# Performance work log

Hardware: AMD Instinct MI355X
Metric: run time of the kernel (lower is better)

## Reference

```python
import jax, jax.numpy as jnp
import numpy as np

B, S, HID = 1, 2048, 2048
H, KV, D = 16, 4, 128
N_REP = H // KV
WINDOW = 1024
THETA = 10000.0
EPS = 1e-6
SCALE = D ** -0.5


def setup_inputs() -> dict:
    key = jax.random.key(0)
    ks = jax.random.split(key, 10)
    s = 0.02
    return {
        "hidden_states": jax.random.normal(ks[0], (B, S, HID), jnp.float32),
        "Wq": jax.random.normal(ks[1], (HID, H * D), jnp.float32) * s,
        "bq": jnp.zeros((H * D,), jnp.float32),
        "Wk": jax.random.normal(ks[2], (HID, KV * D), jnp.float32) * s,
        "bk": jnp.zeros((KV * D,), jnp.float32),
        "Wv": jax.random.normal(ks[3], (HID, KV * D), jnp.float32) * s,
        "bv": jnp.zeros((KV * D,), jnp.float32),
        "Wo": jax.random.normal(ks[4], (H * D, HID), jnp.float32) * s,
        "memory_gate": jnp.zeros((1, H, 1, 1), jnp.float32),
    }


def _rope_tables(seq_len, dim, dtype):
    inv_freq = 1.0 / (THETA ** (jnp.arange(0, dim, 2, dtype=jnp.float32) / dim))
    t = jnp.arange(seq_len, dtype=jnp.float32)
    freqs = t[:, None] * inv_freq[None, :]          # [S, D/2]
    emb = jnp.concatenate([freqs, freqs], axis=-1)  # [S, D]
    return jnp.cos(emb).astype(dtype), jnp.sin(emb).astype(dtype)


def _rotate_half(x):
    x1, x2 = x[..., : x.shape[-1] // 2], x[..., x.shape[-1] // 2 :]
    return jnp.concatenate([-x2, x1], axis=-1)


def reference(hidden_states, Wq, bq, Wk, bk, Wv, bv, Wo, memory_gate):
    b, s, _ = hidden_states.shape
    q = (hidden_states @ Wq + bq).reshape(b, s, H, D).transpose(0, 2, 1, 3)   # [B,H,S,D]
    k = (hidden_states @ Wk + bk).reshape(b, s, KV, D).transpose(0, 2, 1, 3)  # [B,KV,S,D]
    v = (hidden_states @ Wv + bv).reshape(b, s, KV, D).transpose(0, 2, 1, 3)

    cos, sin = _rope_tables(s, D, q.dtype)  # [S,D]
    cos = cos[None, None]                   # [1,1,S,D]
    sin = sin[None, None]
    q_rot = q * cos + _rotate_half(q) * sin
    k_rot = k * cos + _rotate_half(k) * sin

    # GQA repeat of rotated K and raw V to H heads
    k_rep = jnp.repeat(k_rot, N_REP, axis=1)  # [B,H,S,D]
    v_rep = jnp.repeat(v, N_REP, axis=1)

    # sliding-window causal attention (seq_len > window path)
    scores = jnp.einsum("bhsd,bhtd->bhst", q_rot, k_rep) * SCALE
    row = jnp.arange(s)[:, None]
    col = jnp.arange(s)[None, :]
    mask = (col <= row) & (row - col < WINDOW)  # [S,S]
    scores = jnp.where(mask[None, None], scores, -jnp.inf)
    probs = jax.nn.softmax(scores.astype(jnp.float32), axis=-1).astype(q.dtype)
    local = jnp.einsum("bhst,bhtd->bhsd", probs, v_rep)

    # infini-memory retrieval: memory is reset before retrieve, so M=0, z=0
    sigma_q = jax.nn.elu(q) + 1.0                        # unrotated (NoPE) query
    M = jnp.zeros((b, H, D, D), q.dtype)
    z = jnp.zeros((b, H, D), q.dtype)
    num = jnp.einsum("bhsd,bhde->bhse", sigma_q, M)
    den = jnp.einsum("bhsd,bhd->bhs", sigma_q, z) + EPS
    global_out = num / den[..., None]                    # zeros, but faithful math

    gate = jax.nn.sigmoid(memory_gate)                   # [1,H,1,1]
    out = gate * global_out + (1.0 - gate) * local       # [B,H,S,D]
    out = out.transpose(0, 2, 1, 3).reshape(b, s, H * D)
    return out @ Wo
```

## Files before the change

### kernel.cpp

```cpp
#include <hip/hip_runtime.h>
#include <stdint.h>

typedef __attribute__((ext_vector_type(8))) short short8;
typedef __attribute__((ext_vector_type(4))) float f32x4;

#define S_LEN 2048
#define HID 2048
#define NH 16
#define NKV 4
#define DH 128
#define WINDOW 1024
#define SCALE 0.08838834764831845f

__device__ __forceinline__ unsigned short f2bf(float f) {
    unsigned int u = __float_as_uint(f);
    unsigned int r = (u + 0x7fffu + ((u >> 16) & 1u)) >> 16;
    return (unsigned short)r;
}

__device__ __forceinline__ float bf2f(unsigned short u) {
    return __uint_as_float((unsigned int)u << 16);
}

__device__ __forceinline__ void gload16(const void* g, void* l) {
    __builtin_amdgcn_global_load_lds((__attribute__((address_space(1))) void*)g,
                                     (__attribute__((address_space(3))) void*)l, 16, 0, 0);
}


__global__ __launch_bounds__(256) void cast4_kernel(const float* __restrict__ src,
                                                    unsigned short* __restrict__ dst, int n4) {
    int i = blockIdx.x * 256 + threadIdx.x;
    if (i < n4) {
        float4 v = ((const float4*)src)[i];
        ushort4 o;
        o.x = f2bf(v.x); o.y = f2bf(v.y); o.z = f2bf(v.z); o.w = f2bf(v.w);
        ((ushort4*)dst)[i] = o;
    }
}

__global__ __launch_bounds__(256) void build_bias_kernel(const float* __restrict__ bq,
                                                         const float* __restrict__ bk,
                                                         const float* __restrict__ bv,
                                                         float* __restrict__ cbias) {
    int i = blockIdx.x * 256 + threadIdx.x;
    if (i < 3072) {
        float v;
        if (i < 2048) v = bq[i];
        else if (i < 2560) v = bk[i - 2048];
        else v = bv[i - 2560];
        cbias[i] = v;
    }
}

__global__ __launch_bounds__(256) void transpose_cast_kernel(const float* __restrict__ src,
                                                             unsigned short* __restrict__ dst,
                                                             int N, int K, int rowoff) {
    __shared__ unsigned short t[32][33];
    int n0 = blockIdx.x * 32, k0 = blockIdx.y * 32;
    int c = threadIdx.x & 31, r8 = threadIdx.x >> 5;
#pragma unroll
    for (int i = 0; i < 4; i++) {
        int r = r8 + i * 8;
        t[r][c] = f2bf(src[(size_t)(k0 + r) * N + n0 + c]);
    }
    __syncthreads();
#pragma unroll
    for (int i = 0; i < 4; i++) {
        int r = r8 + i * 8;
        dst[(size_t)(rowoff + n0 + r) * K + k0 + c] = t[c][r];
    }
}


template <bool BF16OUT>
__global__ __launch_bounds__(256) void gemm_pipe(const unsigned short* __restrict__ A,
                                                 const unsigned short* __restrict__ Bt,
                                                 void* __restrict__ Cv,
                                                 const float* __restrict__ bias,
                                                 int M, int N, int K) {
    __shared__ unsigned short Al[3][128 * 32];
    __shared__ unsigned short Bl[3][128 * 32];
    const int tid = threadIdx.x, lane = tid & 63, w = tid >> 6;
    const int lo = lane & 15, hi = lane >> 4;
    const int nbn = N >> 7;
    const int nwg8 = gridDim.x >> 3;
    const int wg = (blockIdx.x & 7) * nwg8 + (blockIdx.x >> 3);
    const int bm = wg / nbn, bn = wg % nbn;
    const int m0 = bm << 7, n0 = bn << 7;
    const int wr = w >> 1, wc = w & 1;
    const size_t Kb = (size_t)K * 2;

    const char* Ab = (const char*)A + (size_t)m0 * Kb;
    const char* Bb = (const char*)Bt + (size_t)n0 * Kb;
    char* Alb = (char*)&Al[0][0];
    char* Blb = (char*)&Bl[0][0];

    const int L0 = tid * 16;
    const int L1 = 4096 + tid * 16;
    const int r0 = L0 >> 6, r1 = L1 >> 6;
    const size_t go0 = (size_t)r0 * Kb + ((((L0 >> 4) & 3) ^ (r0 & 3)) << 4);
    const size_t go1 = (size_t)r1 * Kb + ((((L1 >> 4) & 3) ^ (r1 & 3)) << 4);

    auto stage = [&](int buf, int kt) {
        const char* Ak = Ab + (size_t)kt * 64;
        const char* Bk = Bb + (size_t)kt * 64;
        char* Ad = Alb + buf * 8192;
        char* Bd = Blb + buf * 8192;
        gload16(Ak + go0, Ad + L0);
        gload16(Ak + go1, Ad + L1);
        gload16(Bk + go0, Bd + L0);
        gload16(Bk + go1, Bd + L1);
    };

    f32x4 acc[4][4] = {};
    const int NT = K >> 5;
    const int swz = (hi ^ (lo & 3)) << 4;

    stage(0, 0);
    stage(1, 1);
    int buf = 0, nstage = 2;
    for (int kt = 0; kt < NT; ++kt) {
        if (kt < NT - 1)
            asm volatile("s_waitcnt vmcnt(4)" ::: "memory");
        else
            asm volatile("s_waitcnt vmcnt(0)" ::: "memory");
        __builtin_amdgcn_s_barrier();

        const char* Ar = Alb + buf * 8192;
        const char* Br = Blb + buf * 8192;
        short8 af[4], bfr[4];
#pragma unroll
        for (int m = 0; m < 4; m++)
            af[m] = *(const short8*)(Ar + (wr * 64 + m * 16 + lo) * 64 + swz);
#pragma unroll
        for (int n = 0; n < 4; n++)
            bfr[n] = *(const short8*)(Br + (wc * 64 + n * 16 + lo) * 64 + swz);
        asm volatile("s_waitcnt lgkmcnt(0)" ::: "memory");
        __builtin_amdgcn_s_barrier();

        if (kt + 2 < NT) {
            int bst = nstage;
            bst = (bst >= 3) ? bst - 3 : bst;
            stage(bst, kt + 2);
            nstage = bst + 1;
        }
        __builtin_amdgcn_sched_barrier(0);

        __builtin_amdgcn_s_setprio(1);
#pragma unroll
        for (int m = 0; m < 4; m++)
#pragma unroll
            for (int n = 0; n < 4; n++)
                acc[m][n] = __builtin_amdgcn_mfma_f32_16x16x32_bf16(af[m], bfr[n], acc[m][n], 0, 0, 0);
        __builtin_amdgcn_s_setprio(0);

        buf = (buf == 2) ? 0 : buf + 1;
    }

#pragma unroll
    for (int m = 0; m < 4; m++) {
        const int row = m0 + wr * 64 + m * 16 + hi * 4;
#pragma unroll
        for (int n = 0; n < 4; n++) {
            const int col = n0 + wc * 64 + n * 16 + lo;
            const float badd = bias ? bias[col] : 0.f;
#pragma unroll
            for (int r = 0; r < 4; r++) {
                const float v = acc[m][n][r] + badd;
                if constexpr (BF16OUT)
                    ((unsigned short*)Cv)[(size_t)(row + r) * N + col] = f2bf(v);
                else
                    ((float*)Cv)[(size_t)(row + r) * N + col] = v;
            }
        }
    }
}

__global__ __launch_bounds__(256) void rope_qk_kernel(const unsigned short* __restrict__ qkv,
                                                      unsigned short* __restrict__ Qr,
                                                      unsigned short* __restrict__ Kr) {
    int s = blockIdx.x, tid = threadIdx.x;
    __shared__ float cs[64], sn[64];
    if (tid < 64) {
        float inv = __expf(-(float)tid * (logf(10000.f) / 64.f));
        float ang = (float)s * inv;
        float si, co;
        sincosf(ang, &si, &co);
        cs[tid] = co;
        sn[tid] = si;
    }
    __syncthreads();
    const unsigned short* row = qkv + (size_t)s * 3072;
#pragma unroll
    for (int it = 0; it < 8; ++it) {
        int j = tid + it * 256;
        int h = j >> 7, d = j & 127, f = d & 63;
        float x = bf2f(row[j]);
        float other = bf2f(row[(j & ~127) + (d ^ 64)]);
        float v = (d < 64) ? x * cs[f] - other * sn[f] : x * cs[f] + other * sn[f];
        Qr[((size_t)h * S_LEN + s) * 128 + d] = f2bf(v);
    }
#pragma unroll
    for (int it = 0; it < 2; ++it) {
        int j = tid + it * 256;
        int kvh = j >> 7, d = j & 127, f = d & 63;
        float x = bf2f(row[2048 + j]);
        float other = bf2f(row[2048 + (j & ~127) + (d ^ 64)]);
        float v = (d < 64) ? x * cs[f] - other * sn[f] : x * cs[f] + other * sn[f];
        Kr[((size_t)kvh * S_LEN + s) * 128 + d] = f2bf(v);
    }
}

__global__ __launch_bounds__(256) void transpose_v_kernel(const unsigned short* __restrict__ qkv,
                                                          unsigned short* __restrict__ Vt) {
    __shared__ unsigned short t[128][132];
    const int s0 = blockIdx.x * 128;
    const int kvh = blockIdx.y;
    const int tx = threadIdx.x & 15, ty = threadIdx.x >> 4;
    const unsigned short* src = qkv + 2560 + kvh * 128;
#pragma unroll
    for (int i = 0; i < 8; i++) {
        const int sl = ty + i * 16;
        short8 v = *(const short8*)(src + (size_t)(s0 + sl) * 3072 + tx * 8);
#pragma unroll
        for (int j = 0; j < 8; j++) t[sl][tx * 8 + j] = v[j];
    }
    __syncthreads();
    unsigned short* dst = Vt + (size_t)kvh * 128 * S_LEN + s0;
#pragma unroll
    for (int i = 0; i < 8; i++) {
        const int d = ty + i * 16;
        short8 v;
#pragma unroll
        for (int j = 0; j < 8; j++) v[j] = t[tx * 8 + j][d];
        *(short8*)(dst + (size_t)d * S_LEN + tx * 8) = v;
    }
}


__global__ __launch_bounds__(256) void attn_kernel(const unsigned short* __restrict__ Qr,
                                                   const unsigned short* __restrict__ Kr,
                                                   const unsigned short* __restrict__ Vt,
                                                   const float* __restrict__ mg,
                                                   unsigned short* __restrict__ Ao) {
    __shared__ unsigned short Kl[2][64 * 128];
    __shared__ unsigned short Vl[2][128 * 64];
    __shared__ unsigned short Pl[4][16 * 64];
    const int tid = threadIdx.x, lane = tid & 63, w = tid >> 6;
    const int h = blockIdx.y, qt = blockIdx.x;
    const int kvh = h >> 2;
    const int q0 = qt * 64;
    const int lo = lane & 15, hi = lane >> 4;

    const unsigned short* Qb =
        Qr + ((size_t)h * S_LEN + q0 + w * 16 + lo) * 128 + hi * 8;
    short8 qf[4];
#pragma unroll
    for (int ks = 0; ks < 4; ++ks) qf[ks] = *(const short8*)(Qb + ks * 32);

    const float gate = 1.f / (1.f + __expf(-mg[h]));
    const float fac = 1.f - gate;

    float mrow[4] = {-INFINITY, -INFINITY, -INFINITY, -INFINITY};
    float lrow[4] = {0.f, 0.f, 0.f, 0.f};
    f32x4 o[8] = {};

    const char* Kg = (const char*)(Kr + (size_t)kvh * S_LEN * 128);
    const char* Vg = (const char*)(Vt + (size_t)kvh * 128 * S_LEN);
    char* Klb = (char*)&Kl[0][0];
    char* Vlb = (char*)&Vl[0][0];
    const int wb = w * 1024;

    auto stage = [&](int buf, int kt) {
        const int k0 = kt * 64;
#pragma unroll
        for (int iss = 0; iss < 4; ++iss) {
            int lin = iss * 4096 + tid * 16;
            int row = lin >> 8;
            int chunk = (lin >> 4) & 15;
            gload16(Kg + (size_t)(k0 + row) * 256 + ((chunk ^ (row & 7)) << 4),
                    Klb + buf * 16384 + iss * 4096 + wb);
            int d = lin >> 7;
            int vchunk = (lin >> 4) & 7;
            gload16(Vg + (size_t)d * (S_LEN * 2) + (size_t)k0 * 2 + ((vchunk ^ (d & 7)) << 4),
                    Vlb + buf * 16384 + iss * 4096 + wb);
        }
    };

    const int qmin = q0 + w * 16;
    const int t0 = (q0 >= 1023) ? (q0 - 1023) >> 6 : 0;
    stage(0, t0);
    for (int kt = t0; kt <= qt; ++kt) {
        __syncthreads();
        if (kt < qt) stage((kt - t0 + 1) & 1, kt + 1);
        const int buf = (kt - t0) & 1;
        const int k0 = kt * 64;
        const char* Kb = Klb + buf * 16384;
        const char* Vb = Vlb + buf * 16384;

        f32x4 sc[4];
        __builtin_amdgcn_s_setprio(1);
#pragma unroll
        for (int t = 0; t < 4; t++) {
            sc[t] = (f32x4){0.f, 0.f, 0.f, 0.f};
            const int krow = t * 16 + lo;
#pragma unroll
            for (int ks = 0; ks < 4; ks++) {
                const int chunk = ks * 4 + hi;
                short8 kf = *(const short8*)(Kb + krow * 256 + ((chunk ^ (krow & 7)) << 4));
                sc[t] = __builtin_amdgcn_mfma_f32_16x16x32_bf16(qf[ks], kf, sc[t], 0, 0, 0);
            }
        }
        __builtin_amdgcn_s_setprio(0);

        const bool full = (k0 + 63 <= qmin) && (k0 >= qmin + 15 - (WINDOW - 1));
        float ps[4][4];
        float mt[4];
        if (full) {
#pragma unroll
            for (int r = 0; r < 4; r++) {
                float m0v = -INFINITY;
#pragma unroll
                for (int t = 0; t < 4; t++) {
                    float sv = sc[t][r] * SCALE;
                    ps[t][r] = sv;
                    m0v = fmaxf(m0v, sv);
                }
                mt[r] = m0v;
            }
        } else {
#pragma unroll
            for (int r = 0; r < 4; r++) {
                const int q = qmin + hi * 4 + r;
                float m0v = -INFINITY;
#pragma unroll
                for (int t = 0; t < 4; t++) {
                    const int k = k0 + t * 16 + lo;
                    const bool valid = (k <= q) && (q - k < WINDOW);
                    float sv = valid ? sc[t][r] * SCALE : -INFINITY;
                    ps[t][r] = sv;
                    m0v = fmaxf(m0v, sv);
                }
                mt[r] = m0v;
            }
        }

        float alpha[4];
        bool need = false;
#pragma unroll
        for (int r = 0; r < 4; r++) {
#pragma unroll
            for (int off = 1; off < 16; off <<= 1) mt[r] = fmaxf(mt[r], __shfl_xor(mt[r], off, 64));
            const float mo = mrow[r];
            const float mn = (mt[r] > mo + 8.f) ? mt[r] : mo;
            const bool resc = (mn != mo);
            alpha[r] = resc ? __expf(mo - mn) : 1.f;
            need = need || resc;
            mrow[r] = mn;
            const float mn_e = (mn == -INFINITY) ? 0.f : mn;
            float ls = 0.f;
#pragma unroll
            for (int t = 0; t < 4; t++) {
                float p = __expf(ps[t][r] - mn_e);
                ps[t][r] = p;
                ls += p;
            }
#pragma unroll
            for (int off = 1; off < 16; off <<= 1) ls += __shfl_xor(ls, off, 64);
            lrow[r] = lrow[r] * alpha[r] + ls;
        }

        char* Pw = (char*)&Pl[w][0];
#pragma unroll
        for (int r = 0; r < 4; r++) {
            const int prow = hi * 4 + r;
#pragma unroll
            for (int t = 0; t < 4; t++) {
                const int col = t * 16 + lo;
                const int chunk = col >> 3;
                *(unsigned short*)(Pw + prow * 128 + ((chunk ^ (prow & 7)) << 4) + (col & 7) * 2) =
                    f2bf(ps[t][r]);
            }
        }
        asm volatile("s_waitcnt lgkmcnt(0)" ::: "memory");
        __builtin_amdgcn_sched_barrier(0);

        if (__any(need)) {
#pragma unroll
            for (int n = 0; n < 8; n++)
#pragma unroll
                for (int r = 0; r < 4; r++) o[n][r] *= alpha[r];
        }

        short8 pa[2];
#pragma unroll
        for (int ks = 0; ks < 2; ++ks) {
            const int chunk = ks * 4 + hi;
            pa[ks] = *(const short8*)(Pw + lo * 128 + ((chunk ^ (lo & 7)) << 4));
        }

        __builtin_amdgcn_s_setprio(1);
#pragma unroll
        for (int n = 0; n < 8; n++) {
            const int d = n * 16 + lo;
#pragma unroll
            for (int ks = 0; ks < 2; ++ks) {
                const int chunk = ks * 4 + hi;
                short8 vbf = *(const short8*)(Vb + d * 128 + ((chunk ^ (d & 7)) << 4));
                o[n] = __builtin_amdgcn_mfma_f32_16x16x32_bf16(pa[ks], vbf, o[n], 0, 0, 0);
            }
        }
        __builtin_amdgcn_s_setprio(0);
        __syncthreads();
    }

#pragma unroll
    for (int r = 0; r < 4; r++) {
        const int s = q0 + w * 16 + hi * 4 + r;
        const float inv = fac / lrow[r];
#pragma unroll
        for (int n = 0; n < 8; n++) {
            const int d = n * 16 + lo;
            Ao[(size_t)s * 2048 + h * 128 + d] = f2bf(o[n][r] * inv);
        }
    }
}


extern "C" void kernel_launch(void* const* d_in, const int* in_sizes, int n_in,
                              void* d_out, int out_size, void* d_ws, size_t ws_size,
                              hipStream_t stream) {
    const float* hs = (const float*)d_in[0];
    const float* Wq = (const float*)d_in[1];
    const float* bq = (const float*)d_in[2];
    const float* Wk = (const float*)d_in[3];
    const float* bk = (const float*)d_in[4];
    const float* Wv = (const float*)d_in[5];
    const float* bv = (const float*)d_in[6];
    const float* Wo = (const float*)d_in[7];
    const float* mg = (const float*)d_in[8];

    char* ws = (char*)d_ws;
    unsigned short* hsb   = (unsigned short*)(ws + 0);
    unsigned short* woT   = (unsigned short*)(ws + 0);
    unsigned short* wqkvT = (unsigned short*)(ws + 8388608);
    unsigned short* attnb = (unsigned short*)(ws + 8388608);
    unsigned short* qkvb  = (unsigned short*)(ws + 20971520);
    unsigned short* Qrb   = (unsigned short*)(ws + 33554432);
    unsigned short* Krb   = (unsigned short*)(ws + 41943040);
    unsigned short* Vtb   = (unsigned short*)(ws + 44040192);
    float*          cbias = (float*)(ws + 46137344);

    cast4_kernel<<<4096, 256, 0, stream>>>(hs, hsb, 1048576);
    build_bias_kernel<<<12, 256, 0, stream>>>(bq, bk, bv, cbias);
    transpose_cast_kernel<<<dim3(64, 64), 256, 0, stream>>>(Wq, wqkvT, 2048, 2048, 0);
    transpose_cast_kernel<<<dim3(16, 64), 256, 0, stream>>>(Wk, wqkvT, 512, 2048, 2048);
    transpose_cast_kernel<<<dim3(16, 64), 256, 0, stream>>>(Wv, wqkvT, 512, 2048, 2560);

    gemm_pipe<true><<<16 * 24, 256, 0, stream>>>(hsb, wqkvT, qkvb, cbias, 2048, 3072, 2048);

    transpose_cast_kernel<<<dim3(64, 64), 256, 0, stream>>>(Wo, woT, 2048, 2048, 0);

    rope_qk_kernel<<<2048, 256, 0, stream>>>(qkvb, Qrb, Krb);
    transpose_v_kernel<<<dim3(16, 4), 256, 0, stream>>>(qkvb, Vtb);

    attn_kernel<<<dim3(32, 16), 256, 0, stream>>>(Qrb, Krb, Vtb, mg, attnb);

    gemm_pipe<false><<<16 * 16, 256, 0, stream>>>(attnb, woT, (float*)d_out, nullptr, 2048, 2048, 2048);
}
```

Baseline: 254.5 us.

## Merge prep kernels and fuse RoPE and V transpose into QKV GEMM epilogue

All the casting, bias-gathering and weight-transposing kernels are merged into one prep kernel, which also precomputes RoPE cos/sin tables. The QKV GEMM warp layout changes so each warp owns full 128-wide head columns. This lets its epilogue apply bias and RoPE directly, writing rotated Q/K and transposed V, and removes the intermediate qkv buffer plus two kernels. In attention, the softmax row sum is now computed by an MFMA against a ones vector instead of shuffle reductions. The trade-offs are more register pressure in the GEMM epilogue, scattered stores, and a changed warp tiling that reloads all B fragments per warp.

```diff
diff --git a/kernel.cpp b/kernel.cpp
--- a/kernel.cpp
+++ b/kernel.cpp
@@ -18,47 +18,19 @@
     return (unsigned short)r;
 }
 
-__device__ __forceinline__ float bf2f(unsigned short u) {
-    return __uint_as_float((unsigned int)u << 16);
-}
-
 __device__ __forceinline__ void gload16(const void* g, void* l) {
     __builtin_amdgcn_global_load_lds((__attribute__((address_space(1))) void*)g,
                                      (__attribute__((address_space(3))) void*)l, 16, 0, 0);
 }
 
 
-__global__ __launch_bounds__(256) void cast4_kernel(const float* __restrict__ src,
-                                                    unsigned short* __restrict__ dst, int n4) {
-    int i = blockIdx.x * 256 + threadIdx.x;
-    if (i < n4) {
-        float4 v = ((const float4*)src)[i];
-        ushort4 o;
-        o.x = f2bf(v.x); o.y = f2bf(v.y); o.z = f2bf(v.z); o.w = f2bf(v.w);
-        ((ushort4*)dst)[i] = o;
-    }
-}
-
-__global__ __launch_bounds__(256) void build_bias_kernel(const float* __restrict__ bq,
-                                                         const float* __restrict__ bk,
-                                                         const float* __restrict__ bv,
-                                                         float* __restrict__ cbias) {
-    int i = blockIdx.x * 256 + threadIdx.x;
-    if (i < 3072) {
-        float v;
-        if (i < 2048) v = bq[i];
-        else if (i < 2560) v = bk[i - 2048];
-        else v = bv[i - 2560];
-        cbias[i] = v;
-    }
-}
-
-__global__ __launch_bounds__(256) void transpose_cast_kernel(const float* __restrict__ src,
-                                                             unsigned short* __restrict__ dst,
-                                                             int N, int K, int rowoff) {
-    __shared__ unsigned short t[32][33];
-    int n0 = blockIdx.x * 32, k0 = blockIdx.y * 32;
-    int c = threadIdx.x & 31, r8 = threadIdx.x >> 5;
+__device__ __forceinline__ void tile_transpose(const float* __restrict__ src,
+                                               unsigned short* __restrict__ dst,
+                                               int N, int K, int rowoff, int idx, int nbx,
+                                               unsigned short (*t)[33]) {
+    const int nx = idx & (nbx - 1), ky = idx / nbx;
+    const int n0 = nx * 32, k0 = ky * 32;
+    const int c = threadIdx.x & 31, r8 = threadIdx.x >> 5;
 #pragma unroll
     for (int i = 0; i < 4; i++) {
         int r = r8 + i * 8;
@@ -72,13 +44,58 @@
     }
 }
 
-
-template <bool BF16OUT>
-__global__ __launch_bounds__(256) void gemm_pipe(const unsigned short* __restrict__ A,
-                                                 const unsigned short* __restrict__ Bt,
-                                                 void* __restrict__ Cv,
-                                                 const float* __restrict__ bias,
-                                                 int M, int N, int K) {
+__global__ __launch_bounds__(256) void prep_kernel(
+    const float* __restrict__ hs, unsigned short* __restrict__ hsb,
+    const float* __restrict__ bq, const float* __restrict__ bk, const float* __restrict__ bv,
+    float* __restrict__ cbias, float* __restrict__ cst, float* __restrict__ snt,
+    const float* __restrict__ Wq, const float* __restrict__ Wk,
+    const float* __restrict__ Wv, const float* __restrict__ Wo,
+    unsigned short* __restrict__ wqkvT, unsigned short* __restrict__ woT) {
+    __shared__ unsigned short t[32][33];
+    const int b = blockIdx.x, tid = threadIdx.x;
+    if (b < 4096) {
+        int i = b * 256 + tid;
+        float4 v = ((const float4*)hs)[i];
+        ushort4 o;
+        o.x = f2bf(v.x); o.y = f2bf(v.y); o.z = f2bf(v.z); o.w = f2bf(v.w);
+        ((ushort4*)hsb)[i] = o;
+    } else if (b < 4608) {
+        int idx = (b - 4096) * 256 + tid;
+        int s = idx >> 6, f = idx & 63;
+        float inv = __expf(-(float)f * (logf(10000.f) / 64.f));
+        float ang = (float)s * inv;
+        float si, co;
+        sincosf(ang, &si, &co);
+        cst[idx] = co;
+        snt[idx] = si;
+    } else if (b < 4620) {
+        int i = (b - 4608) * 256 + tid;
+        if (i < 3072) {
+            float v;
+            if (i < 2048) v = bq[i];
+            else if (i < 2560) v = bk[i - 2048];
+            else v = bv[i - 2560];
+            cbias[i] = v;
+        }
+    } else if (b < 8716) {
+        tile_transpose(Wq, wqkvT, 2048, 2048, 0, b - 4620, 64, t);
+    } else if (b < 9740) {
+        tile_transpose(Wk, wqkvT, 512, 2048, 2048, b - 8716, 16, t);
+    } else if (b < 10764) {
+        tile_transpose(Wv, wqkvT, 512, 2048, 2560, b - 9740, 16, t);
+    } else {
+        tile_transpose(Wo, woT, 2048, 2048, 0, b - 10764, 64, t);
+    }
+}
+
+
+template <int EPI>
+__global__ __launch_bounds__(256) void gemm_pipe(
+    const unsigned short* __restrict__ A, const unsigned short* __restrict__ Bt,
+    float* __restrict__ C, const float* __restrict__ bias, int M, int N, int K,
+    unsigned short* __restrict__ Qr, unsigned short* __restrict__ Kr,
+    unsigned short* __restrict__ Vt,
+    const float* __restrict__ cst, const float* __restrict__ snt) {
     __shared__ unsigned short Al[3][128 * 32];
     __shared__ unsigned short Bl[3][128 * 32];
     const int tid = threadIdx.x, lane = tid & 63, w = tid >> 6;
@@ -88,7 +105,6 @@
     const int wg = (blockIdx.x & 7) * nwg8 + (blockIdx.x >> 3);
     const int bm = wg / nbn, bn = wg % nbn;
     const int m0 = bm << 7, n0 = bn << 7;
-    const int wr = w >> 1, wc = w & 1;
     const size_t Kb = (size_t)K * 2;
 
     const char* Ab = (const char*)A + (size_t)m0 * Kb;
@@ -113,7 +129,7 @@
         gload16(Bk + go1, Bd + L1);
     };
 
-    f32x4 acc[4][4] = {};
+    f32x4 acc[2][8] = {};
     const int NT = K >> 5;
     const int swz = (hi ^ (lo & 3)) << 4;
 
@@ -129,13 +145,13 @@
 
         const char* Ar = Alb + buf * 8192;
         const char* Br = Blb + buf * 8192;
-        short8 af[4], bfr[4];
-#pragma unroll
-        for (int m = 0; m < 4; m++)
-            af[m] = *(const short8*)(Ar + (wr * 64 + m * 16 + lo) * 64 + swz);
-#pragma unroll
-        for (int n = 0; n < 4; n++)
-            bfr[n] = *(const short8*)(Br + (wc * 64 + n * 16 + lo) * 64 + swz);
+        short8 af[2], bfr[8];
+#pragma unroll
+        for (int m = 0; m < 2; m++)
+            af[m] = *(const short8*)(Ar + (w * 32 + m * 16 + lo) * 64 + swz);
+#pragma unroll
+        for (int n = 0; n < 8; n++)
+            bfr[n] = *(const short8*)(Br + (n * 16 + lo) * 64 + swz);
         asm volatile("s_waitcnt lgkmcnt(0)" ::: "memory");
         __builtin_amdgcn_s_barrier();
 
@@ -149,92 +165,83 @@
 
         __builtin_amdgcn_s_setprio(1);
 #pragma unroll
-        for (int m = 0; m < 4; m++)
-#pragma unroll
-            for (int n = 0; n < 4; n++)
+        for (int m = 0; m < 2; m++)
+#pragma unroll
+            for (int n = 0; n < 8; n++)
                 acc[m][n] = __builtin_amdgcn_mfma_f32_16x16x32_bf16(af[m], bfr[n], acc[m][n], 0, 0, 0);
         __builtin_amdgcn_s_setprio(0);
 
         buf = (buf == 2) ? 0 : buf + 1;
     }
 
-#pragma unroll
-    for (int m = 0; m < 4; m++) {
-        const int row = m0 + wr * 64 + m * 16 + hi * 4;
-#pragma unroll
-        for (int n = 0; n < 4; n++) {
-            const int col = n0 + wc * 64 + n * 16 + lo;
-            const float badd = bias ? bias[col] : 0.f;
-#pragma unroll
-            for (int r = 0; r < 4; r++) {
-                const float v = acc[m][n][r] + badd;
-                if constexpr (BF16OUT)
-                    ((unsigned short*)Cv)[(size_t)(row + r) * N + col] = f2bf(v);
-                else
-                    ((float*)Cv)[(size_t)(row + r) * N + col] = v;
-            }
-        }
-    }
-}
-
-__global__ __launch_bounds__(256) void rope_qk_kernel(const unsigned short* __restrict__ qkv,
-                                                      unsigned short* __restrict__ Qr,
-                                                      unsigned short* __restrict__ Kr) {
-    int s = blockIdx.x, tid = threadIdx.x;
-    __shared__ float cs[64], sn[64];
-    if (tid < 64) {
-        float inv = __expf(-(float)tid * (logf(10000.f) / 64.f));
-        float ang = (float)s * inv;
-        float si, co;
-        sincosf(ang, &si, &co);
-        cs[tid] = co;
-        sn[tid] = si;
-    }
-    __syncthreads();
-    const unsigned short* row = qkv + (size_t)s * 3072;
-#pragma unroll
-    for (int it = 0; it < 8; ++it) {
-        int j = tid + it * 256;
-        int h = j >> 7, d = j & 127, f = d & 63;
-        float x = bf2f(row[j]);
-        float other = bf2f(row[(j & ~127) + (d ^ 64)]);
-        float v = (d < 64) ? x * cs[f] - other * sn[f] : x * cs[f] + other * sn[f];
-        Qr[((size_t)h * S_LEN + s) * 128 + d] = f2bf(v);
-    }
-#pragma unroll
-    for (int it = 0; it < 2; ++it) {
-        int j = tid + it * 256;
-        int kvh = j >> 7, d = j & 127, f = d & 63;
-        float x = bf2f(row[2048 + j]);
-        float other = bf2f(row[2048 + (j & ~127) + (d ^ 64)]);
-        float v = (d < 64) ? x * cs[f] - other * sn[f] : x * cs[f] + other * sn[f];
-        Kr[((size_t)kvh * S_LEN + s) * 128 + d] = f2bf(v);
-    }
-}
-
-__global__ __launch_bounds__(256) void transpose_v_kernel(const unsigned short* __restrict__ qkv,
-                                                          unsigned short* __restrict__ Vt) {
-    __shared__ unsigned short t[128][132];
-    const int s0 = blockIdx.x * 128;
-    const int kvh = blockIdx.y;
-    const int tx = threadIdx.x & 15, ty = threadIdx.x >> 4;
-    const unsigned short* src = qkv + 2560 + kvh * 128;
-#pragma unroll
-    for (int i = 0; i < 8; i++) {
-        const int sl = ty + i * 16;
-        short8 v = *(const short8*)(src + (size_t)(s0 + sl) * 3072 + tx * 8);
-#pragma unroll
-        for (int j = 0; j < 8; j++) t[sl][tx * 8 + j] = v[j];
-    }
-    __syncthreads();
-    unsigned short* dst = Vt + (size_t)kvh * 128 * S_LEN + s0;
-#pragma unroll
-    for (int i = 0; i < 8; i++) {
-        const int d = ty + i * 16;
-        short8 v;
-#pragma unroll
-        for (int j = 0; j < 8; j++) v[j] = t[tx * 8 + j][d];
-        *(short8*)(dst + (size_t)d * S_LEN + tx * 8) = v;
+    const int sbase = m0 + w * 32 + hi * 4;
+    if constexpr (EPI == 0) {
+#pragma unroll
+        for (int m = 0; m < 2; m++) {
+            const int row = sbase + m * 16;
+#pragma unroll
+            for (int n = 0; n < 8; n++) {
+                const int col = n0 + n * 16 + lo;
+                const float badd = bias ? bias[col] : 0.f;
+#pragma unroll
+                for (int r = 0; r < 4; r++)
+                    C[(size_t)(row + r) * N + col] = acc[m][n][r] + badd;
+            }
+        }
+    } else {
+        if (bn < 20) {
+            float csv[2][4][4], snv[2][4][4];
+#pragma unroll
+            for (int m = 0; m < 2; m++)
+#pragma unroll
+                for (int r = 0; r < 4; r++) {
+                    const int s = sbase + m * 16 + r;
+#pragma unroll
+                    for (int fi = 0; fi < 4; fi++) {
+                        const int f = fi * 16 + lo;
+                        csv[m][r][fi] = cst[s * 64 + f];
+                        snv[m][r][fi] = snt[s * 64 + f];
+                    }
+                }
+            unsigned short* dst = (bn < 16) ? (Qr + (size_t)bn * S_LEN * 128)
+                                            : (Kr + (size_t)(bn - 16) * S_LEN * 128);
+#pragma unroll
+            for (int m = 0; m < 2; m++) {
+#pragma unroll
+                for (int n = 0; n < 8; n++) {
+                    const int d = n * 16 + lo;
+                    const float badd = bias[n0 + d];
+                    const float badd2 = bias[n0 + (d ^ 64)];
+#pragma unroll
+                    for (int r = 0; r < 4; r++) {
+                        const float x = acc[m][n][r] + badd;
+                        const float y = acc[m][n ^ 4][r] + badd2;
+                        const float cs = csv[m][r][n & 3];
+                        const float sn = snv[m][r][n & 3];
+                        const float out = (n < 4) ? x * cs - y * sn : x * cs + y * sn;
+                        const int s = sbase + m * 16 + r;
+                        dst[(size_t)s * 128 + d] = f2bf(out);
+                    }
+                }
+            }
+        } else {
+            const int kvh = bn - 20;
+#pragma unroll
+            for (int m = 0; m < 2; m++) {
+                const int s0r = sbase + m * 16;
+#pragma unroll
+                for (int n = 0; n < 8; n++) {
+                    const int d = n * 16 + lo;
+                    const float badd = bias[n0 + d];
+                    ushort4 pk;
+                    pk.x = f2bf(acc[m][n][0] + badd);
+                    pk.y = f2bf(acc[m][n][1] + badd);
+                    pk.z = f2bf(acc[m][n][2] + badd);
+                    pk.w = f2bf(acc[m][n][3] + badd);
+                    *(ushort4*)(Vt + (size_t)(kvh * 128 + d) * S_LEN + s0r) = pk;
+                }
+            }
+        }
     }
 }
 
@@ -262,9 +269,11 @@
     const float gate = 1.f / (1.f + __expf(-mg[h]));
     const float fac = 1.f - gate;
 
+    const short8 ones = {16256, 16256, 16256, 16256, 16256, 16256, 16256, 16256};
+
     float mrow[4] = {-INFINITY, -INFINITY, -INFINITY, -INFINITY};
-    float lrow[4] = {0.f, 0.f, 0.f, 0.f};
     f32x4 o[8] = {};
+    f32x4 ol = {};
 
     const char* Kg = (const char*)(Kr + (size_t)kvh * S_LEN * 128);
     const char* Vg = (const char*)(Vt + (size_t)kvh * 128 * S_LEN);
@@ -359,16 +368,8 @@
             need = need || resc;
             mrow[r] = mn;
             const float mn_e = (mn == -INFINITY) ? 0.f : mn;
-            float ls = 0.f;
-#pragma unroll
-            for (int t = 0; t < 4; t++) {
-                float p = __expf(ps[t][r] - mn_e);
-                ps[t][r] = p;
-                ls += p;
-            }
-#pragma unroll
-            for (int off = 1; off < 16; off <<= 1) ls += __shfl_xor(ls, off, 64);
-            lrow[r] = lrow[r] * alpha[r] + ls;
+#pragma unroll
+            for (int t = 0; t < 4; t++) ps[t][r] = __expf(ps[t][r] - mn_e);
         }
 
         char* Pw = (char*)&Pl[w][0];
@@ -391,6 +392,8 @@
             for (int n = 0; n < 8; n++)
 #pragma unroll
                 for (int r = 0; r < 4; r++) o[n][r] *= alpha[r];
+#pragma unroll
+            for (int r = 0; r < 4; r++) ol[r] *= alpha[r];
         }
 
         short8 pa[2];
@@ -401,6 +404,8 @@
         }
 
         __builtin_amdgcn_s_setprio(1);
+        ol = __builtin_amdgcn_mfma_f32_16x16x32_bf16(pa[0], ones, ol, 0, 0, 0);
+        ol = __builtin_amdgcn_mfma_f32_16x16x32_bf16(pa[1], ones, ol, 0, 0, 0);
 #pragma unroll
         for (int n = 0; n < 8; n++) {
             const int d = n * 16 + lo;
@@ -418,7 +423,7 @@
 #pragma unroll
     for (int r = 0; r < 4; r++) {
         const int s = q0 + w * 16 + hi * 4 + r;
-        const float inv = fac / lrow[r];
+        const float inv = fac / ol[r];
 #pragma unroll
         for (int n = 0; n < 8; n++) {
             const int d = n * 16 + lo;
@@ -443,29 +448,24 @@
 
     char* ws = (char*)d_ws;
     unsigned short* hsb   = (unsigned short*)(ws + 0);
-    unsigned short* woT   = (unsigned short*)(ws + 0);
+    unsigned short* attnb = (unsigned short*)(ws + 0);
     unsigned short* wqkvT = (unsigned short*)(ws + 8388608);
-    unsigned short* attnb = (unsigned short*)(ws + 8388608);
-    unsigned short* qkvb  = (unsigned short*)(ws + 20971520);
-    unsigned short* Qrb   = (unsigned short*)(ws + 33554432);
-    unsigned short* Krb   = (unsigned short*)(ws + 41943040);
-    unsigned short* Vtb   = (unsigned short*)(ws + 44040192);
-    float*          cbias = (float*)(ws + 46137344);
-
-    cast4_kernel<<<4096, 256, 0, stream>>>(hs, hsb, 1048576);
-    build_bias_kernel<<<12, 256, 0, stream>>>(bq, bk, bv, cbias);
-    transpose_cast_kernel<<<dim3(64, 64), 256, 0, stream>>>(Wq, wqkvT, 2048, 2048, 0);
-    transpose_cast_kernel<<<dim3(16, 64), 256, 0, stream>>>(Wk, wqkvT, 512, 2048, 2048);
-    transpose_cast_kernel<<<dim3(16, 64), 256, 0, stream>>>(Wv, wqkvT, 512, 2048, 2560);
-
-    gemm_pipe<true><<<16 * 24, 256, 0, stream>>>(hsb, wqkvT, qkvb, cbias, 2048, 3072, 2048);
-
-    transpose_cast_kernel<<<dim3(64, 64), 256, 0, stream>>>(Wo, woT, 2048, 2048, 0);
-
-    rope_qk_kernel<<<2048, 256, 0, stream>>>(qkvb, Qrb, Krb);
-    transpose_v_kernel<<<dim3(16, 4), 256, 0, stream>>>(qkvb, Vtb);
+    unsigned short* woT   = (unsigned short*)(ws + 20971520);
+    unsigned short* Qrb   = (unsigned short*)(ws + 29360128);
+    unsigned short* Krb   = (unsigned short*)(ws + 37748736);
+    unsigned short* Vtb   = (unsigned short*)(ws + 39845888);
+    float*          cbias = (float*)(ws + 41943040);
+    float*          cst   = (float*)(ws + 41959424);
+    float*          snt   = (float*)(ws + 42483712);
+
+    prep_kernel<<<14860, 256, 0, stream>>>(hs, hsb, bq, bk, bv, cbias, cst, snt,
+                                           Wq, Wk, Wv, Wo, wqkvT, woT);
+
+    gemm_pipe<1><<<16 * 24, 256, 0, stream>>>(hsb, wqkvT, nullptr, cbias, 2048, 3072, 2048,
+                                              Qrb, Krb, Vtb, cst, snt);
 
     attn_kernel<<<dim3(32, 16), 256, 0, stream>>>(Qrb, Krb, Vtb, mg, attnb);
 
-    gemm_pipe<false><<<16 * 16, 256, 0, stream>>>(attnb, woT, (float*)d_out, nullptr, 2048, 2048, 2048);
-}
+    gemm_pipe<0><<<16 * 16, 256, 0, stream>>>(attnb, woT, (float*)d_out, nullptr, 2048, 2048, 2048,
+                                              nullptr, nullptr, nullptr, nullptr, nullptr);
+}
```

Measured after the change: 235.1 us. 1.08x faster.
